# Optimization experiments

Measured on AMD Instinct MI355X. Metric: run time of the kernel, lower is better.

## Reference

```python
import jax, jax.numpy as jnp
import numpy as np

B, C2D, C3D, NC = 8, 256, 512, 128
H = W = 64
T = H3 = W3 = 16


def setup_inputs() -> dict:
    key = jax.random.key(0)
    ks = jax.random.split(key, 12)
    s = 0.02
    return {
        "features_2d": jax.random.normal(ks[0], (B, C2D, H, W), jnp.float32),
        "features_3d": jax.random.normal(ks[1], (B, C3D, T, H3, W3), jnp.float32),
        "Wq": jax.random.normal(ks[2], (NC, C2D), jnp.float32) * s,
        "bq": jax.random.normal(ks[3], (NC,), jnp.float32) * s,
        "Wk": jax.random.normal(ks[4], (NC, C3D), jnp.float32) * s,
        "bk": jax.random.normal(ks[5], (NC,), jnp.float32) * s,
        "Wv": jax.random.normal(ks[6], (NC, C3D), jnp.float32) * s,
        "bv": jax.random.normal(ks[7], (NC,), jnp.float32) * s,
        "Wo": jax.random.normal(ks[8], (C2D, NC), jnp.float32) * s,
        "bo": jax.random.normal(ks[9], (C2D,), jnp.float32) * s,
        "Wps": jax.random.normal(ks[10], (C2D, C2D, 3, 3), jnp.float32) * s,
        "bps": jax.random.normal(ks[11], (C2D,), jnp.float32) * s,
    }


def reference(features_2d, features_3d, Wq, bq, Wk, bk, Wv, bv, Wo, bo, Wps, bps):
    # 1x1 conv Q over 2D features: [B, NC, H*W] -> [B, N2d, NC]
    Q = jnp.einsum("bchw,oc->bohw", features_2d, Wq) + bq[None, :, None, None]
    Q = Q.reshape(B, NC, H * W).transpose(0, 2, 1)          # [B, N2d, NC]
    # 1x1 conv K/V over 3D features (no pooling: H3 <= max_height_3d)
    K = jnp.einsum("bcthw,oc->bothw", features_3d, Wk) + bk[None, :, None, None, None]
    V = jnp.einsum("bcthw,oc->bothw", features_3d, Wv) + bv[None, :, None, None, None]
    K = K.reshape(B, NC, T * H3 * W3)                        # [B, NC, N3d]
    V = V.reshape(B, NC, T * H3 * W3).transpose(0, 2, 1)     # [B, N3d, NC]
    # full non-local attention (no 1/sqrt(d) scaling, matching the torch code)
    att = jnp.einsum("bnc,bcm->bnm", Q, K)                   # [B, N2d, N3d]
    att = jax.nn.softmax(att, axis=-1)
    out = jnp.einsum("bnm,bmc->bnc", att, V)                 # [B, N2d, NC]
    out = out.transpose(0, 2, 1).reshape(B, NC, H, W)
    # 1x1 output conv back to channels_2d
    out = jnp.einsum("bchw,oc->bohw", out, Wo) + bo[None, :, None, None]
    # residual add + 3x3 post-sum conv
    x = features_2d + out
    y = jax.lax.conv_general_dilated(
        x, Wps, window_strides=(1, 1), padding="SAME",
        dimension_numbers=("NCHW", "OIHW", "NCHW"))
    return y + bps[None, :, None, None]
```

## Files before the change

kernel.cpp:

```cpp
#include <hip/hip_runtime.h>
#include <cstdint>

#define NB  8
#define C2  256
#define C3  512
#define NCH 128
#define NN2 4096
#define NN3 4096

using f4 = float4;
typedef float f32x16 __attribute__((ext_vector_type(16)));
typedef __bf16 bf16x8 __attribute__((ext_vector_type(8)));

union FragU {
    uint4    q;
    uint32_t u[4];
    bf16x8   v;
};

__device__ __forceinline__ void fma4(float* acc, float a, const f4 w) {
    acc[0] = fmaf(a, w.x, acc[0]);
    acc[1] = fmaf(a, w.y, acc[1]);
    acc[2] = fmaf(a, w.z, acc[2]);
    acc[3] = fmaf(a, w.w, acc[3]);
}

__device__ __forceinline__ unsigned short f2bf(float f) {
    uint32_t u = __float_as_uint(f);
    u += 0x7fffu + ((u >> 16) & 1u);
    return (unsigned short)(u >> 16);
}
__device__ __forceinline__ float bf2f(unsigned short h) {
    return __uint_as_float(((uint32_t)h) << 16);
}
__device__ __forceinline__ uint32_t pkbf(float lo, float hi) {
    union { __bf16 h[2]; uint32_t u; } t;
    t.h[0] = (__bf16)lo;
    t.h[1] = (__bf16)hi;
    return t.u;
}

__global__ __launch_bounds__(256) void wprep(const float* __restrict__ Wps,
                                             unsigned short* __restrict__ Wb) {
    int idx = blockIdx.x * 256 + threadIdx.x;
    int t = idx >> 16;
    int r = idx & 65535;
    int co = r >> 8, ci = r & 255;
    Wb[idx] = f2bf(Wps[((size_t)(co * 256 + ci)) * 9 + t]);
}

__global__ __launch_bounds__(256) void proj_q(const float* __restrict__ f2d,
                                              const float* __restrict__ Wq,
                                              const float* __restrict__ bq,
                                              unsigned short* __restrict__ Q) {
    __shared__ __align__(16) float As[32 * 68];
    __shared__ __align__(16) float Ws[32 * 132];
    const int tid = threadIdx.x;
    const int b  = blockIdx.x >> 6;
    const int n0 = (blockIdx.x & 63) << 6;
    const int tx = tid & 15, ty = tid >> 4;
    float acc[4][2][4];
#pragma unroll
    for (int i = 0; i < 4; i++)
#pragma unroll
        for (int v = 0; v < 2; v++)
#pragma unroll
            for (int u = 0; u < 4; u++) acc[i][v][u] = 0.f;
    const float* Ab = f2d + (size_t)b * C2 * NN2 + n0;
    for (int k0 = 0; k0 < C2; k0 += 32) {
#pragma unroll
        for (int i = 0; i < 2; i++) {
            int cidx = tid + 256 * i;
            int kk = cidx >> 4, noff = (cidx & 15) << 2;
            *(f4*)(As + kk * 68 + noff) = *(const f4*)(Ab + (size_t)(k0 + kk) * NN2 + noff);
        }
#pragma unroll
        for (int i = 0; i < 4; i++) {
            int cidx = tid + 256 * i;
            int cc = cidx >> 3, koff = (cidx & 7) << 2;
            f4 w = *(const f4*)(Wq + cc * C2 + k0 + koff);
            Ws[(koff + 0) * 132 + cc] = w.x;
            Ws[(koff + 1) * 132 + cc] = w.y;
            Ws[(koff + 2) * 132 + cc] = w.z;
            Ws[(koff + 3) * 132 + cc] = w.w;
        }
        __syncthreads();
#pragma unroll 8
        for (int kk = 0; kk < 32; kk++) {
            f4 a4 = *(const f4*)(As + kk * 68 + 4 * ty);
            f4 w0 = *(const f4*)(Ws + kk * 132 + 4 * tx);
            f4 w1 = *(const f4*)(Ws + kk * 132 + 4 * tx + 64);
            float av[4] = {a4.x, a4.y, a4.z, a4.w};
#pragma unroll
            for (int i = 0; i < 4; i++) { fma4(acc[i][0], av[i], w0); fma4(acc[i][1], av[i], w1); }
        }
        __syncthreads();
    }
    f4 b0 = *(const f4*)(bq + 4 * tx);
    f4 b1 = *(const f4*)(bq + 4 * tx + 64);
    float ba[2][4] = {{b0.x, b0.y, b0.z, b0.w}, {b1.x, b1.y, b1.z, b1.w}};
#pragma unroll
    for (int i = 0; i < 4; i++) {
        unsigned short* row = Q + ((size_t)b * NN2 + n0 + 4 * ty + i) * NCH;
#pragma unroll
        for (int v = 0; v < 2; v++) {
            ushort4 r;
            r.x = f2bf(acc[i][v][0] + ba[v][0]);
            r.y = f2bf(acc[i][v][1] + ba[v][1]);
            r.z = f2bf(acc[i][v][2] + ba[v][2]);
            r.w = f2bf(acc[i][v][3] + ba[v][3]);
            *(ushort4*)(row + 4 * tx + 64 * v) = r;
        }
    }
}

__global__ __launch_bounds__(256) void proj_kv(const float* __restrict__ f3d,
                                               const float* __restrict__ Wk,
                                               const float* __restrict__ bk,
                                               const float* __restrict__ Wv,
                                               const float* __restrict__ bv,
                                               unsigned short* __restrict__ K,
                                               unsigned short* __restrict__ Vt) {
    __shared__ __align__(16) float smem[2176 + 4224 + 4224];
    float* As  = smem;
    float* Wks = smem + 2176;
    float* Wvs = smem + 2176 + 4224;
    const int tid = threadIdx.x;
    const int b  = blockIdx.x >> 6;
    const int n0 = (blockIdx.x & 63) << 6;
    const int tx = tid & 15, ty = tid >> 4;
    float acck[4][2][4], accv[4][2][4];
#pragma unroll
    for (int i = 0; i < 4; i++)
#pragma unroll
        for (int v = 0; v < 2; v++)
#pragma unroll
            for (int u = 0; u < 4; u++) { acck[i][v][u] = 0.f; accv[i][v][u] = 0.f; }
    const float* Ab = f3d + (size_t)b * C3 * NN3 + n0;
    for (int k0 = 0; k0 < C3; k0 += 32) {
#pragma unroll
        for (int i = 0; i < 2; i++) {
            int cidx = tid + 256 * i;
            int kk = cidx >> 4, noff = (cidx & 15) << 2;
            *(f4*)(As + kk * 68 + noff) = *(const f4*)(Ab + (size_t)(k0 + kk) * NN3 + noff);
        }
#pragma unroll
        for (int i = 0; i < 4; i++) {
            int cidx = tid + 256 * i;
            int cc = cidx >> 3, koff = (cidx & 7) << 2;
            f4 wkv = *(const f4*)(Wk + cc * C3 + k0 + koff);
            Wks[(koff + 0) * 132 + cc] = wkv.x;
            Wks[(koff + 1) * 132 + cc] = wkv.y;
            Wks[(koff + 2) * 132 + cc] = wkv.z;
            Wks[(koff + 3) * 132 + cc] = wkv.w;
            f4 wvv = *(const f4*)(Wv + cc * C3 + k0 + koff);
            Wvs[(koff + 0) * 132 + cc] = wvv.x;
            Wvs[(koff + 1) * 132 + cc] = wvv.y;
            Wvs[(koff + 2) * 132 + cc] = wvv.z;
            Wvs[(koff + 3) * 132 + cc] = wvv.w;
        }
        __syncthreads();
#pragma unroll 4
        for (int kk = 0; kk < 32; kk++) {
            f4 a4  = *(const f4*)(As + kk * 68 + 4 * ty);
            f4 k0v = *(const f4*)(Wks + kk * 132 + 4 * tx);
            f4 k1v = *(const f4*)(Wks + kk * 132 + 4 * tx + 64);
            f4 v0v = *(const f4*)(Wvs + kk * 132 + 4 * tx);
            f4 v1v = *(const f4*)(Wvs + kk * 132 + 4 * tx + 64);
            float av[4] = {a4.x, a4.y, a4.z, a4.w};
#pragma unroll
            for (int i = 0; i < 4; i++) {
                fma4(acck[i][0], av[i], k0v); fma4(acck[i][1], av[i], k1v);
                fma4(accv[i][0], av[i], v0v); fma4(accv[i][1], av[i], v1v);
            }
        }
        __syncthreads();
    }
    f4 bk0 = *(const f4*)(bk + 4 * tx);
    f4 bk1 = *(const f4*)(bk + 4 * tx + 64);
    f4 bv0 = *(const f4*)(bv + 4 * tx);
    f4 bv1 = *(const f4*)(bv + 4 * tx + 64);
    float bka[2][4] = {{bk0.x, bk0.y, bk0.z, bk0.w}, {bk1.x, bk1.y, bk1.z, bk1.w}};
    float bva[2][4] = {{bv0.x, bv0.y, bv0.z, bv0.w}, {bv1.x, bv1.y, bv1.z, bv1.w}};
#pragma unroll
    for (int i = 0; i < 4; i++) {
        unsigned short* row = K + ((size_t)b * NN3 + n0 + 4 * ty + i) * NCH;
#pragma unroll
        for (int v = 0; v < 2; v++) {
            ushort4 r;
            r.x = f2bf(acck[i][v][0] + bka[v][0]);
            r.y = f2bf(acck[i][v][1] + bka[v][1]);
            r.z = f2bf(acck[i][v][2] + bka[v][2]);
            r.w = f2bf(acck[i][v][3] + bka[v][3]);
            *(ushort4*)(row + 4 * tx + 64 * v) = r;
        }
    }
    unsigned short* vt = (unsigned short*)smem;
#pragma unroll
    for (int i = 0; i < 4; i++) {
        int ml = 4 * ty + i;
#pragma unroll
        for (int v = 0; v < 2; v++)
#pragma unroll
            for (int u = 0; u < 4; u++) {
                int c = 4 * tx + 64 * v + u;
                vt[c * 72 + ml] = f2bf(accv[i][v][u] + bva[v][u]);
            }
    }
    __syncthreads();
#pragma unroll
    for (int j = 0; j < 4; j++) {
        int idx = tid + 256 * j;
        int c = idx >> 3, gm = idx & 7;
        uint4 d = *(const uint4*)(vt + c * 72 + gm * 8);
        *(uint4*)(Vt + ((size_t)b * NCH + c) * NN3 + n0 + gm * 8) = d;
    }
}

__global__ __launch_bounds__(128, 1) void attn(const unsigned short* __restrict__ Qg,
                                               const unsigned short* __restrict__ Kg,
                                               const unsigned short* __restrict__ Vtg,
                                               unsigned short* __restrict__ AO) {
    __shared__ __align__(16) unsigned short Ks[2][64 * 128];
    __shared__ __align__(16) unsigned short Vs[2][128 * 64];
    const int tid = threadIdx.x;
    const int b  = blockIdx.x >> 6;
    const int qc = blockIdx.x & 63;
    const int lane = tid & 63;
    const int wid = tid >> 6;
    const int i31 = lane & 31;
    const int h   = lane >> 5;
    const int q0w = qc * 64 + wid * 32;

    uint4 qf[8];
    const unsigned short* Qrow = Qg + ((size_t)b * NN2 + q0w + i31) * NCH;
#pragma unroll
    for (int dc = 0; dc < 8; dc++) qf[dc] = *(const uint4*)(Qrow + dc * 16 + h * 8);

    f32x16 o[4];
#pragma unroll
    for (int cf = 0; cf < 4; cf++)
#pragma unroll
        for (int r = 0; r < 16; r++) o[cf][r] = 0.f;
    float m_run = -3.0e38f, l_run = 0.f;

    const unsigned short* Kb = Kg  + (size_t)b * NN3 * NCH;
    const unsigned short* Vb = Vtg + (size_t)b * NCH * NN3;

    uint4 kst[8], vst[8];
#pragma unroll
    for (int j = 0; j < 8; j++) {
        int idx = tid + 128 * j;
        int key = idx >> 4, g = idx & 15;
        kst[j] = *(const uint4*)(Kb + (size_t)key * NCH + g * 8);
        int c = idx >> 3, gm = idx & 7;
        vst[j] = *(const uint4*)(Vb + (size_t)c * NN3 + gm * 8);
    }
#pragma unroll
    for (int j = 0; j < 8; j++) {
        int idx = tid + 128 * j;
        int key = idx >> 4, g = idx & 15;
        *(uint4*)(&Ks[0][key * 128 + ((g ^ (key & 7)) * 8)]) = kst[j];
        int c = idx >> 3, gm = idx & 7;
        *(uint4*)(&Vs[0][c * 64 + ((gm ^ (c & 7)) * 8)]) = vst[j];
    }
    __syncthreads();

    int buf = 0;
    for (int t = 0; t < 64; t++) {
        const bool more = (t + 1 < 64);
        const int m0n = more ? (t + 1) * 64 : 0;
        if (more) {
#pragma unroll
            for (int j = 0; j < 8; j++) {
                int idx = tid + 128 * j;
                int key = idx >> 4, g = idx & 15;
                kst[j] = *(const uint4*)(Kb + (size_t)(m0n + key) * NCH + g * 8);
                int c = idx >> 3, gm = idx & 7;
                vst[j] = *(const uint4*)(Vb + (size_t)c * NN3 + m0n + gm * 8);
            }
        }
        f32x16 sacc[2];
#pragma unroll
        for (int kf = 0; kf < 2; kf++)
#pragma unroll
            for (int r = 0; r < 16; r++) sacc[kf][r] = 0.f;
#pragma unroll
        for (int dc = 0; dc < 8; dc++) {
            FragU bq; bq.q = qf[dc];
#pragma unroll
            for (int kf = 0; kf < 2; kf++) {
                FragU ak;
                ak.q = *(const uint4*)(&Ks[buf][(kf * 32 + i31) * 128 + (((2 * dc + h) ^ (i31 & 7)) * 8)]);
                sacc[kf] = __builtin_amdgcn_mfma_f32_32x32x16_bf16(ak.v, bq.v, sacc[kf], 0, 0, 0);
            }
        }
        float tmax = -3.0e38f;
#pragma unroll
        for (int kf = 0; kf < 2; kf++)
#pragma unroll
            for (int r = 0; r < 16; r++) tmax = fmaxf(tmax, sacc[kf][r]);
        tmax = fmaxf(tmax, __shfl_xor(tmax, 32, 64));
        if (__any(tmax > m_run)) {
            float newm = fmaxf(m_run, tmax);
            float scale = __expf(m_run - newm);
            m_run = newm;
            l_run *= scale;
#pragma unroll
            for (int reg = 0; reg < 16; reg++) {
                int qrow = (reg & 3) + 8 * (reg >> 2) + 4 * h;
                float sc = __shfl(scale, qrow, 64);
#pragma unroll
                for (int cf = 0; cf < 4; cf++) o[cf][reg] *= sc;
            }
        }
        float psum = 0.f;
#pragma unroll
        for (int kf = 0; kf < 2; kf++)
#pragma unroll
            for (int r = 0; r < 16; r++) {
                float e = __expf(sacc[kf][r] - m_run);
                sacc[kf][r] = e;
                psum += e;
            }
        psum += __shfl_xor(psum, 32, 64);
        l_run += psum;
        uint32_t pk[2][8];
#pragma unroll
        for (int kf = 0; kf < 2; kf++)
#pragma unroll
            for (int j = 0; j < 8; j++) pk[kf][j] = pkbf(sacc[kf][2 * j], sacc[kf][2 * j + 1]);
#pragma unroll
        for (int kc = 0; kc < 4; kc++) {
            const int kf = kc >> 1, kcp = kc & 1;
            uint32_t own_lo  = pk[kf][4 * kcp + 0];
            uint32_t own_lo2 = pk[kf][4 * kcp + 1];
            uint32_t own_hi  = pk[kf][4 * kcp + 2];
            uint32_t own_hi2 = pk[kf][4 * kcp + 3];
            uint32_t send1 = h ? own_lo  : own_hi;
            uint32_t send2 = h ? own_lo2 : own_hi2;
            uint32_t recv1 = (uint32_t)__shfl_xor((int)send1, 32, 64);
            uint32_t recv2 = (uint32_t)__shfl_xor((int)send2, 32, 64);
            FragU pa;
            pa.u[0] = h ? recv1 : own_lo;
            pa.u[1] = h ? recv2 : own_lo2;
            pa.u[2] = h ? own_hi  : recv1;
            pa.u[3] = h ? own_hi2 : recv2;
#pragma unroll
            for (int cf = 0; cf < 4; cf++) {
                FragU vbf;
                vbf.q = *(const uint4*)(&Vs[buf][(cf * 32 + i31) * 64 + (((2 * kc + h) ^ (i31 & 7)) * 8)]);
                o[cf] = __builtin_amdgcn_mfma_f32_32x32x16_bf16(pa.v, vbf.v, o[cf], 0, 0, 0);
            }
        }
        if (more) {
#pragma unroll
            for (int j = 0; j < 8; j++) {
                int idx = tid + 128 * j;
                int key = idx >> 4, g = idx & 15;
                *(uint4*)(&Ks[buf ^ 1][key * 128 + ((g ^ (key & 7)) * 8)]) = kst[j];
                int c = idx >> 3, gm = idx & 7;
                *(uint4*)(&Vs[buf ^ 1][c * 64 + ((gm ^ (c & 7)) * 8)]) = vst[j];
            }
        }
        __syncthreads();
        buf ^= 1;
    }
    float inv = 1.0f / l_run;
#pragma unroll
    for (int reg = 0; reg < 16; reg++) {
        int qrow = (reg & 3) + 8 * (reg >> 2) + 4 * h;
        float iv = __shfl(inv, qrow, 64);
        unsigned short* row = AO + ((size_t)b * NN2 + q0w + qrow) * NCH;
#pragma unroll
        for (int cf = 0; cf < 4; cf++) row[cf * 32 + i31] = f2bf(o[cf][reg] * iv);
    }
}

__global__ __launch_bounds__(256) void outproj(const unsigned short* __restrict__ AO,
                                               const float* __restrict__ Wo,
                                               const float* __restrict__ bo,
                                               const float* __restrict__ f2d,
                                               unsigned short* __restrict__ Xn) {
    __shared__ __align__(16) float smem[2176 + 4224];
    float* Wt = smem;
    float* At = smem + 2176;
    const int tid = threadIdx.x;
    const int b = blockIdx.x >> 7;
    const int r = blockIdx.x & 127;
    const int co0 = (r >> 5) << 6;
    const int n0  = (r & 31) << 7;
    const int tx = tid & 15, ty = tid >> 4;
    float acc[4][2][4];
#pragma unroll
    for (int i = 0; i < 4; i++)
#pragma unroll
        for (int v = 0; v < 2; v++)
#pragma unroll
            for (int u = 0; u < 4; u++) acc[i][v][u] = 0.f;
    for (int c0 = 0; c0 < NCH; c0 += 32) {
#pragma unroll
        for (int i = 0; i < 2; i++) {
            int cidx = tid + 256 * i;
            int cr = cidx >> 3, koff = (cidx & 7) << 2;
            f4 w = *(const f4*)(Wo + (co0 + cr) * NCH + c0 + koff);
            Wt[(koff + 0) * 68 + cr] = w.x;
            Wt[(koff + 1) * 68 + cr] = w.y;
            Wt[(koff + 2) * 68 + cr] = w.z;
            Wt[(koff + 3) * 68 + cr] = w.w;
        }
#pragma unroll
        for (int i = 0; i < 4; i++) {
            int cidx = tid + 256 * i;
            int nn = cidx >> 3, koff = (cidx & 7) << 2;
            ushort4 a4 = *(const ushort4*)(AO + ((size_t)b * NN2 + n0 + nn) * NCH + c0 + koff);
            At[(koff + 0) * 132 + nn] = bf2f(a4.x);
            At[(koff + 1) * 132 + nn] = bf2f(a4.y);
            At[(koff + 2) * 132 + nn] = bf2f(a4.z);
            At[(koff + 3) * 132 + nn] = bf2f(a4.w);
        }
        __syncthreads();
#pragma unroll 8
        for (int kk = 0; kk < 32; kk++) {
            f4 a4 = *(const f4*)(Wt + kk * 68 + 4 * ty);
            f4 x0 = *(const f4*)(At + kk * 132 + 4 * tx);
            f4 x1 = *(const f4*)(At + kk * 132 + 4 * tx + 64);
            float av[4] = {a4.x, a4.y, a4.z, a4.w};
#pragma unroll
            for (int i = 0; i < 4; i++) { fma4(acc[i][0], av[i], x0); fma4(acc[i][1], av[i], x1); }
        }
        __syncthreads();
    }
    unsigned short* tb = (unsigned short*)smem;
#pragma unroll
    for (int i = 0; i < 4; i++) {
        int co = co0 + 4 * ty + i;
        float bias = bo[co];
        const size_t rowb = ((size_t)b * C2 + co) * NN2 + n0;
#pragma unroll
        for (int v = 0; v < 2; v++) {
            size_t pidx = rowb + 4 * tx + 64 * v;
            f4 f = *(const f4*)(f2d + pidx);
            int nl = 4 * tx + 64 * v;
            tb[(nl + 0) * 72 + 4 * ty + i] = f2bf(acc[i][v][0] + bias + f.x);
            tb[(nl + 1) * 72 + 4 * ty + i] = f2bf(acc[i][v][1] + bias + f.y);
            tb[(nl + 2) * 72 + 4 * ty + i] = f2bf(acc[i][v][2] + bias + f.z);
            tb[(nl + 3) * 72 + 4 * ty + i] = f2bf(acc[i][v][3] + bias + f.w);
        }
    }
    __syncthreads();
#pragma unroll
    for (int k = 0; k < 4; k++) {
        int unit = tid + 256 * k;
        int nl = unit >> 3, cc = unit & 7;
        uint4 d = *(const uint4*)(tb + nl * 72 + cc * 8);
        *(uint4*)(Xn + ((size_t)b * NN2 + n0 + nl) * C2 + co0 + cc * 8) = d;
    }
}

__global__ __launch_bounds__(256) void conv3x3(const unsigned short* __restrict__ Xn,
                                               const unsigned short* __restrict__ Wb,
                                               const float* __restrict__ bps,
                                               float* __restrict__ Y) {
    __shared__ __align__(16) unsigned short Xs[680 * 8];
    const int tid = threadIdx.x;
    const int b  = blockIdx.x >> 6;
    const int r  = blockIdx.x & 63;
    const int ct = r >> 4;
    const int pt = r & 15;
    const int px0 = (pt & 1) << 5;
    const int py0 = (pt >> 1) << 3;
    const int w    = tid >> 6;
    const int lane = tid & 63;
    const int i31  = lane & 31;
    const int h    = lane >> 5;
    const int co0  = ct << 6;

    f32x16 acc[2][2];
#pragma unroll
    for (int ch = 0; ch < 2; ch++)
#pragma unroll
        for (int pf = 0; pf < 2; pf++)
#pragma unroll
            for (int q = 0; q < 16; q++) acc[ch][pf][q] = 0.f;

    const unsigned short* Xb = Xn + (size_t)b * NN2 * C2;

    uint4 sreg[3];
    int su[3], sy[3], sx[3], sh[3];
#pragma unroll
    for (int k = 0; k < 3; k++) {
        int u = tid + 256 * k;
        su[k] = (u < 680);
        int pix = u >> 1;
        sy[k] = pix / 34;
        sx[k] = pix - sy[k] * 34;
        sh[k] = u & 1;
    }

    auto stage_load = [&](int ci0) {
#pragma unroll
        for (int k = 0; k < 3; k++) {
            uint4 z = {0, 0, 0, 0};
            if (su[k]) {
                int gy = py0 - 1 + sy[k];
                int gx = px0 - 1 + sx[k];
                if ((unsigned)gy < 64u && (unsigned)gx < 64u)
                    z = *(const uint4*)(Xb + ((size_t)(gy * 64 + gx)) * C2 + ci0 + 8 * sh[k]);
            }
            sreg[k] = z;
        }
    };
    auto stage_write = [&]() {
#pragma unroll
        for (int k = 0; k < 3; k++) {
            if (su[k]) {
                int slot = (sy[k] * 2 + sh[k]) * 34 + sx[k];
                *(uint4*)(&Xs[slot * 8]) = sreg[k];
            }
        }
    };

    stage_load(0);
    stage_write();
    __syncthreads();

    for (int c = 0; c < 16; c++) {
        const int ci0n = (c + 1) * 16;
        if (c + 1 < 16) stage_load(ci0n);
        const int ci0 = c * 16;
#pragma unroll
        for (int t = 0; t < 9; t++) {
            const int dy = t / 3, dx = t - dy * 3;
            FragU a0, a1;
            a0.q = *(const uint4*)(Wb + ((size_t)(t * 256 + co0 + i31)) * 256 + ci0 + 8 * h);
            a1.q = *(const uint4*)(Wb + ((size_t)(t * 256 + co0 + 32 + i31)) * 256 + ci0 + 8 * h);
#pragma unroll
            for (int pf = 0; pf < 2; pf++) {
                const int yl = 2 * w + pf;
                FragU bx;
                bx.q = *(const uint4*)(&Xs[(((yl + dy) * 2 + h) * 34 + i31 + dx) * 8]);
                acc[0][pf] = __builtin_amdgcn_mfma_f32_32x32x16_bf16(a0.v, bx.v, acc[0][pf], 0, 0, 0);
                acc[1][pf] = __builtin_amdgcn_mfma_f32_32x32x16_bf16(a1.v, bx.v, acc[1][pf], 0, 0, 0);
            }
        }
        __syncthreads();
        if (c + 1 < 16) stage_write();
        __syncthreads();
    }

#pragma unroll
    for (int ch = 0; ch < 2; ch++)
#pragma unroll
        for (int pf = 0; pf < 2; pf++) {
            const int y = py0 + 2 * w + pf;
            const int x = px0 + i31;
#pragma unroll
            for (int q = 0; q < 16; q++) {
                int co = co0 + ch * 32 + (q & 3) + 8 * (q >> 2) + 4 * h;
                Y[(((size_t)b * C2 + co) * 64 + y) * 64 + x] = acc[ch][pf][q] + bps[co];
            }
        }
}

extern "C" void kernel_launch(void* const* d_in, const int* in_sizes, int n_in,
                              void* d_out, int out_size, void* d_ws, size_t ws_size,
                              hipStream_t stream) {
    const float* f2d = (const float*)d_in[0];
    const float* f3d = (const float*)d_in[1];
    const float* Wq  = (const float*)d_in[2];
    const float* bq  = (const float*)d_in[3];
    const float* Wk  = (const float*)d_in[4];
    const float* bk  = (const float*)d_in[5];
    const float* Wv  = (const float*)d_in[6];
    const float* bv  = (const float*)d_in[7];
    const float* Wo  = (const float*)d_in[8];
    const float* bo  = (const float*)d_in[9];
    const float* Wps = (const float*)d_in[10];
    const float* bps = (const float*)d_in[11];
    float* Y = (float*)d_out;

    unsigned short* Qb  = (unsigned short*)d_ws;
    unsigned short* Kb  = Qb + 4194304;
    unsigned short* Vtb = Kb + 4194304;
    unsigned short* AOb = Vtb + 4194304;
    unsigned short* Xnb = AOb + 4194304;
    unsigned short* Wbb = Xnb + 8388608;

    dim3 blk(256);
    wprep   <<<dim3(2304), blk, 0, stream>>>(Wps, Wbb);
    proj_q  <<<dim3(512),  blk, 0, stream>>>(f2d, Wq, bq, Qb);
    proj_kv <<<dim3(512),  blk, 0, stream>>>(f3d, Wk, bk, Wv, bv, Kb, Vtb);
    attn    <<<dim3(512),  dim3(128), 0, stream>>>(Qb, Kb, Vtb, AOb);
    outproj <<<dim3(1024), blk, 0, stream>>>(AOb, Wo, bo, f2d, Xnb);
    conv3x3 <<<dim3(512),  blk, 0, stream>>>(Xnb, Wbb, bps, Y);
}
```

Measured before the change: 534.4 us.

## Use bf16 MFMA for Q/K/V projections and split attention keys across wave pairs

Replaces the fp32 FMA Q and K/V projection kernels with bf16 MFMA kernels, fed by a new weight-conversion pre-pass and double-buffered LDS staging. The attention kernel moves to 256 threads: two wave pairs each handle half of the key range and are merged at the end with a log-sum-exp combine through shared memory. It also adds s_setprio around the MFMA sections. The aim is to cut projection ALU time and raise attention occupancy and parallelism, at the cost of bf16 rounding of the projection inputs and an extra merge step.

```diff
diff --git a/kernel.cpp b/kernel.cpp
--- a/kernel.cpp
+++ b/kernel.cpp
@@ -18,26 +18,25 @@
     bf16x8   v;
 };
 
+__device__ __forceinline__ unsigned short f2bf(float f) {
+    uint32_t u = __float_as_uint(f);
+    u += 0x7fffu + ((u >> 16) & 1u);
+    return (unsigned short)(u >> 16);
+}
+__device__ __forceinline__ float bf2f(unsigned short h) {
+    return __uint_as_float(((uint32_t)h) << 16);
+}
+__device__ __forceinline__ uint32_t pkbf(float lo, float hi) {
+    union { __bf16 h[2]; uint32_t u; } t;
+    t.h[0] = (__bf16)lo;
+    t.h[1] = (__bf16)hi;
+    return t.u;
+}
 __device__ __forceinline__ void fma4(float* acc, float a, const f4 w) {
     acc[0] = fmaf(a, w.x, acc[0]);
     acc[1] = fmaf(a, w.y, acc[1]);
     acc[2] = fmaf(a, w.z, acc[2]);
     acc[3] = fmaf(a, w.w, acc[3]);
-}
-
-__device__ __forceinline__ unsigned short f2bf(float f) {
-    uint32_t u = __float_as_uint(f);
-    u += 0x7fffu + ((u >> 16) & 1u);
-    return (unsigned short)(u >> 16);
-}
-__device__ __forceinline__ float bf2f(unsigned short h) {
-    return __uint_as_float(((uint32_t)h) << 16);
-}
-__device__ __forceinline__ uint32_t pkbf(float lo, float hi) {
-    union { __bf16 h[2]; uint32_t u; } t;
-    t.h[0] = (__bf16)lo;
-    t.h[1] = (__bf16)hi;
-    return t.u;
 }
 
 __global__ __launch_bounds__(256) void wprep(const float* __restrict__ Wps,
@@ -49,188 +48,205 @@
     Wb[idx] = f2bf(Wps[((size_t)(co * 256 + ci)) * 9 + t]);
 }
 
+__global__ __launch_bounds__(256) void wprep2(const float* __restrict__ Wq,
+                                              const float* __restrict__ Wk,
+                                              const float* __restrict__ Wv,
+                                              unsigned short* __restrict__ Wqb,
+                                              unsigned short* __restrict__ Wkb,
+                                              unsigned short* __restrict__ Wvb) {
+    int idx = blockIdx.x * 256 + threadIdx.x;
+    if (idx < 32768)        Wqb[idx]          = f2bf(Wq[idx]);
+    else if (idx < 98304)   Wkb[idx - 32768]  = f2bf(Wk[idx - 32768]);
+    else                    Wvb[idx - 98304]  = f2bf(Wv[idx - 98304]);
+}
+
 __global__ __launch_bounds__(256) void proj_q(const float* __restrict__ f2d,
-                                              const float* __restrict__ Wq,
+                                              const unsigned short* __restrict__ Wqb,
                                               const float* __restrict__ bq,
                                               unsigned short* __restrict__ Q) {
-    __shared__ __align__(16) float As[32 * 68];
-    __shared__ __align__(16) float Ws[32 * 132];
+    __shared__ __align__(16) unsigned short Xs[2][128 * 40];
     const int tid = threadIdx.x;
-    const int b  = blockIdx.x >> 6;
-    const int n0 = (blockIdx.x & 63) << 6;
-    const int tx = tid & 15, ty = tid >> 4;
-    float acc[4][2][4];
-#pragma unroll
-    for (int i = 0; i < 4; i++)
-#pragma unroll
-        for (int v = 0; v < 2; v++)
-#pragma unroll
-            for (int u = 0; u < 4; u++) acc[i][v][u] = 0.f;
-    const float* Ab = f2d + (size_t)b * C2 * NN2 + n0;
-    for (int k0 = 0; k0 < C2; k0 += 32) {
-#pragma unroll
-        for (int i = 0; i < 2; i++) {
-            int cidx = tid + 256 * i;
-            int kk = cidx >> 4, noff = (cidx & 15) << 2;
-            *(f4*)(As + kk * 68 + noff) = *(const f4*)(Ab + (size_t)(k0 + kk) * NN2 + noff);
-        }
-#pragma unroll
-        for (int i = 0; i < 4; i++) {
-            int cidx = tid + 256 * i;
-            int cc = cidx >> 3, koff = (cidx & 7) << 2;
-            f4 w = *(const f4*)(Wq + cc * C2 + k0 + koff);
-            Ws[(koff + 0) * 132 + cc] = w.x;
-            Ws[(koff + 1) * 132 + cc] = w.y;
-            Ws[(koff + 2) * 132 + cc] = w.z;
-            Ws[(koff + 3) * 132 + cc] = w.w;
-        }
+    const int b  = blockIdx.x >> 5;
+    const int n0 = (blockIdx.x & 31) << 7;
+    const int wn = tid >> 6;
+    const int lane = tid & 63;
+    const int i31 = lane & 31;
+    const int h   = lane >> 5;
+    const int kp = tid >> 4;
+    const int nc = tid & 15;
+
+    f32x16 aQ[4];
+#pragma unroll
+    for (int cf = 0; cf < 4; cf++)
+#pragma unroll
+        for (int r = 0; r < 16; r++) aQ[cf][r] = 0.f;
+
+    float xlo[8], xhi[8];
+    auto LOADC = [&](int k0) {
+        const float* r0 = f2d + ((size_t)b * C2 + k0 + 2 * kp) * NN2 + n0 + nc;
+        const float* r1 = r0 + NN2;
+#pragma unroll
+        for (int i = 0; i < 8; i++) { xlo[i] = r0[16 * i]; xhi[i] = r1[16 * i]; }
+    };
+    auto WRITEC = [&](int bi) {
+        unsigned short* X = Xs[bi];
+#pragma unroll
+        for (int i = 0; i < 8; i++)
+            *(uint32_t*)&X[(nc + 16 * i) * 40 + 2 * kp] = pkbf(xlo[i], xhi[i]);
+    };
+
+    LOADC(0); WRITEC(0); __syncthreads();
+    int cur = 0;
+    for (int c = 0; c < 8; c++) {
+        if (c + 1 < 8) LOADC((c + 1) * 32);
+        const int k0 = c * 32;
+        FragU xf[2];
+        xf[0].q = *(const uint4*)&Xs[cur][(wn * 32 + i31) * 40 + h * 8];
+        xf[1].q = *(const uint4*)&Xs[cur][(wn * 32 + i31) * 40 + 16 + h * 8];
+#pragma unroll
+        for (int ks = 0; ks < 2; ks++) {
+            const int ko = k0 + ks * 16 + h * 8;
+#pragma unroll
+            for (int cf = 0; cf < 4; cf++) {
+                FragU wq;
+                wq.q = *(const uint4*)&Wqb[(size_t)(cf * 32 + i31) * 256 + ko];
+                aQ[cf] = __builtin_amdgcn_mfma_f32_32x32x16_bf16(wq.v, xf[ks].v, aQ[cf], 0, 0, 0);
+            }
+        }
+        if (c + 1 < 8) WRITEC(cur ^ 1);
         __syncthreads();
-#pragma unroll 8
-        for (int kk = 0; kk < 32; kk++) {
-            f4 a4 = *(const f4*)(As + kk * 68 + 4 * ty);
-            f4 w0 = *(const f4*)(Ws + kk * 132 + 4 * tx);
-            f4 w1 = *(const f4*)(Ws + kk * 132 + 4 * tx + 64);
-            float av[4] = {a4.x, a4.y, a4.z, a4.w};
-#pragma unroll
-            for (int i = 0; i < 4; i++) { fma4(acc[i][0], av[i], w0); fma4(acc[i][1], av[i], w1); }
-        }
-        __syncthreads();
-    }
-    f4 b0 = *(const f4*)(bq + 4 * tx);
-    f4 b1 = *(const f4*)(bq + 4 * tx + 64);
-    float ba[2][4] = {{b0.x, b0.y, b0.z, b0.w}, {b1.x, b1.y, b1.z, b1.w}};
-#pragma unroll
-    for (int i = 0; i < 4; i++) {
-        unsigned short* row = Q + ((size_t)b * NN2 + n0 + 4 * ty + i) * NCH;
-#pragma unroll
-        for (int v = 0; v < 2; v++) {
-            ushort4 r;
-            r.x = f2bf(acc[i][v][0] + ba[v][0]);
-            r.y = f2bf(acc[i][v][1] + ba[v][1]);
-            r.z = f2bf(acc[i][v][2] + ba[v][2]);
-            r.w = f2bf(acc[i][v][3] + ba[v][3]);
-            *(ushort4*)(row + 4 * tx + 64 * v) = r;
-        }
-    }
+        cur ^= 1;
+    }
+    const int nQ = n0 + wn * 32 + i31;
+    unsigned short* Qrow = Q + ((size_t)b * NN2 + nQ) * NCH;
+#pragma unroll
+    for (int cf = 0; cf < 4; cf++)
+#pragma unroll
+        for (int tq = 0; tq < 4; tq++) {
+            int c0 = cf * 32 + 8 * tq + 4 * h;
+            f4 bb = *(const f4*)(bq + c0);
+            ushort4 s;
+            s.x = f2bf(aQ[cf][4 * tq + 0] + bb.x);
+            s.y = f2bf(aQ[cf][4 * tq + 1] + bb.y);
+            s.z = f2bf(aQ[cf][4 * tq + 2] + bb.z);
+            s.w = f2bf(aQ[cf][4 * tq + 3] + bb.w);
+            *(ushort4*)(Qrow + c0) = s;
+        }
 }
 
 __global__ __launch_bounds__(256) void proj_kv(const float* __restrict__ f3d,
-                                               const float* __restrict__ Wk,
+                                               const unsigned short* __restrict__ Wkb,
                                                const float* __restrict__ bk,
-                                               const float* __restrict__ Wv,
+                                               const unsigned short* __restrict__ Wvb,
                                                const float* __restrict__ bv,
                                                unsigned short* __restrict__ K,
                                                unsigned short* __restrict__ Vt) {
-    __shared__ __align__(16) float smem[2176 + 4224 + 4224];
-    float* As  = smem;
-    float* Wks = smem + 2176;
-    float* Wvs = smem + 2176 + 4224;
+    __shared__ __align__(16) unsigned short Xs[2][128 * 40];
     const int tid = threadIdx.x;
-    const int b  = blockIdx.x >> 6;
-    const int n0 = (blockIdx.x & 63) << 6;
-    const int tx = tid & 15, ty = tid >> 4;
-    float acck[4][2][4], accv[4][2][4];
-#pragma unroll
-    for (int i = 0; i < 4; i++)
-#pragma unroll
-        for (int v = 0; v < 2; v++)
-#pragma unroll
-            for (int u = 0; u < 4; u++) { acck[i][v][u] = 0.f; accv[i][v][u] = 0.f; }
-    const float* Ab = f3d + (size_t)b * C3 * NN3 + n0;
-    for (int k0 = 0; k0 < C3; k0 += 32) {
-#pragma unroll
-        for (int i = 0; i < 2; i++) {
-            int cidx = tid + 256 * i;
-            int kk = cidx >> 4, noff = (cidx & 15) << 2;
-            *(f4*)(As + kk * 68 + noff) = *(const f4*)(Ab + (size_t)(k0 + kk) * NN3 + noff);
-        }
-#pragma unroll
-        for (int i = 0; i < 4; i++) {
-            int cidx = tid + 256 * i;
-            int cc = cidx >> 3, koff = (cidx & 7) << 2;
-            f4 wkv = *(const f4*)(Wk + cc * C3 + k0 + koff);
-            Wks[(koff + 0) * 132 + cc] = wkv.x;
-            Wks[(koff + 1) * 132 + cc] = wkv.y;
-            Wks[(koff + 2) * 132 + cc] = wkv.z;
-            Wks[(koff + 3) * 132 + cc] = wkv.w;
-            f4 wvv = *(const f4*)(Wv + cc * C3 + k0 + koff);
-            Wvs[(koff + 0) * 132 + cc] = wvv.x;
-            Wvs[(koff + 1) * 132 + cc] = wvv.y;
-            Wvs[(koff + 2) * 132 + cc] = wvv.z;
-            Wvs[(koff + 3) * 132 + cc] = wvv.w;
-        }
+    const int b  = blockIdx.x >> 5;
+    const int n0 = (blockIdx.x & 31) << 7;
+    const int wn = tid >> 6;
+    const int lane = tid & 63;
+    const int i31 = lane & 31;
+    const int h   = lane >> 5;
+    const int kp = tid >> 4;
+    const int nc = tid & 15;
+
+    f32x16 aK[4], aV[4];
+#pragma unroll
+    for (int cf = 0; cf < 4; cf++)
+#pragma unroll
+        for (int r = 0; r < 16; r++) { aK[cf][r] = 0.f; aV[cf][r] = 0.f; }
+
+    float xlo[8], xhi[8];
+    auto LOADC = [&](int k0) {
+        const float* r0 = f3d + ((size_t)b * C3 + k0 + 2 * kp) * NN3 + n0 + nc;
+        const float* r1 = r0 + NN3;
+#pragma unroll
+        for (int i = 0; i < 8; i++) { xlo[i] = r0[16 * i]; xhi[i] = r1[16 * i]; }
+    };
+    auto WRITEC = [&](int bi) {
+        unsigned short* X = Xs[bi];
+#pragma unroll
+        for (int i = 0; i < 8; i++)
+            *(uint32_t*)&X[(nc + 16 * i) * 40 + 2 * kp] = pkbf(xlo[i], xhi[i]);
+    };
+
+    LOADC(0); WRITEC(0); __syncthreads();
+    int cur = 0;
+    for (int c = 0; c < 16; c++) {
+        if (c + 1 < 16) LOADC((c + 1) * 32);
+        const int k0 = c * 32;
+        FragU xf[2];
+        xf[0].q = *(const uint4*)&Xs[cur][(wn * 32 + i31) * 40 + h * 8];
+        xf[1].q = *(const uint4*)&Xs[cur][(wn * 32 + i31) * 40 + 16 + h * 8];
+#pragma unroll
+        for (int ks = 0; ks < 2; ks++) {
+            const int ko = k0 + ks * 16 + h * 8;
+#pragma unroll
+            for (int cf = 0; cf < 4; cf++) {
+                FragU wk, wv;
+                wk.q = *(const uint4*)&Wkb[(size_t)(cf * 32 + i31) * 512 + ko];
+                wv.q = *(const uint4*)&Wvb[(size_t)(cf * 32 + i31) * 512 + ko];
+                aK[cf] = __builtin_amdgcn_mfma_f32_32x32x16_bf16(wk.v, xf[ks].v, aK[cf], 0, 0, 0);
+                aV[cf] = __builtin_amdgcn_mfma_f32_32x32x16_bf16(xf[ks].v, wv.v, aV[cf], 0, 0, 0);
+            }
+        }
+        if (c + 1 < 16) WRITEC(cur ^ 1);
         __syncthreads();
-#pragma unroll 4
-        for (int kk = 0; kk < 32; kk++) {
-            f4 a4  = *(const f4*)(As + kk * 68 + 4 * ty);
-            f4 k0v = *(const f4*)(Wks + kk * 132 + 4 * tx);
-            f4 k1v = *(const f4*)(Wks + kk * 132 + 4 * tx + 64);
-            f4 v0v = *(const f4*)(Wvs + kk * 132 + 4 * tx);
-            f4 v1v = *(const f4*)(Wvs + kk * 132 + 4 * tx + 64);
-            float av[4] = {a4.x, a4.y, a4.z, a4.w};
-#pragma unroll
-            for (int i = 0; i < 4; i++) {
-                fma4(acck[i][0], av[i], k0v); fma4(acck[i][1], av[i], k1v);
-                fma4(accv[i][0], av[i], v0v); fma4(accv[i][1], av[i], v1v);
-            }
-        }
-        __syncthreads();
-    }
-    f4 bk0 = *(const f4*)(bk + 4 * tx);
-    f4 bk1 = *(const f4*)(bk + 4 * tx + 64);
-    f4 bv0 = *(const f4*)(bv + 4 * tx);
-    f4 bv1 = *(const f4*)(bv + 4 * tx + 64);
-    float bka[2][4] = {{bk0.x, bk0.y, bk0.z, bk0.w}, {bk1.x, bk1.y, bk1.z, bk1.w}};
-    float bva[2][4] = {{bv0.x, bv0.y, bv0.z, bv0.w}, {bv1.x, bv1.y, bv1.z, bv1.w}};
-#pragma unroll
-    for (int i = 0; i < 4; i++) {
-        unsigned short* row = K + ((size_t)b * NN3 + n0 + 4 * ty + i) * NCH;
-#pragma unroll
-        for (int v = 0; v < 2; v++) {
-            ushort4 r;
-            r.x = f2bf(acck[i][v][0] + bka[v][0]);
-            r.y = f2bf(acck[i][v][1] + bka[v][1]);
-            r.z = f2bf(acck[i][v][2] + bka[v][2]);
-            r.w = f2bf(acck[i][v][3] + bka[v][3]);
-            *(ushort4*)(row + 4 * tx + 64 * v) = r;
-        }
-    }
-    unsigned short* vt = (unsigned short*)smem;
-#pragma unroll
-    for (int i = 0; i < 4; i++) {
-        int ml = 4 * ty + i;
-#pragma unroll
-        for (int v = 0; v < 2; v++)
-#pragma unroll
-            for (int u = 0; u < 4; u++) {
-                int c = 4 * tx + 64 * v + u;
-                vt[c * 72 + ml] = f2bf(accv[i][v][u] + bva[v][u]);
-            }
-    }
-    __syncthreads();
-#pragma unroll
-    for (int j = 0; j < 4; j++) {
-        int idx = tid + 256 * j;
-        int c = idx >> 3, gm = idx & 7;
-        uint4 d = *(const uint4*)(vt + c * 72 + gm * 8);
-        *(uint4*)(Vt + ((size_t)b * NCH + c) * NN3 + n0 + gm * 8) = d;
-    }
-}
-
-__global__ __launch_bounds__(128, 1) void attn(const unsigned short* __restrict__ Qg,
-                                               const unsigned short* __restrict__ Kg,
-                                               const unsigned short* __restrict__ Vtg,
-                                               unsigned short* __restrict__ AO) {
-    __shared__ __align__(16) unsigned short Ks[2][64 * 128];
-    __shared__ __align__(16) unsigned short Vs[2][128 * 64];
+        cur ^= 1;
+    }
+    const int nK = n0 + wn * 32 + i31;
+    unsigned short* Krow = K + ((size_t)b * NN3 + nK) * NCH;
+#pragma unroll
+    for (int cf = 0; cf < 4; cf++)
+#pragma unroll
+        for (int tq = 0; tq < 4; tq++) {
+            int c0 = cf * 32 + 8 * tq + 4 * h;
+            f4 bb = *(const f4*)(bk + c0);
+            ushort4 s;
+            s.x = f2bf(aK[cf][4 * tq + 0] + bb.x);
+            s.y = f2bf(aK[cf][4 * tq + 1] + bb.y);
+            s.z = f2bf(aK[cf][4 * tq + 2] + bb.z);
+            s.w = f2bf(aK[cf][4 * tq + 3] + bb.w);
+            *(ushort4*)(Krow + c0) = s;
+        }
+#pragma unroll
+    for (int cf = 0; cf < 4; cf++) {
+        const int cV = cf * 32 + i31;
+        const float bvv = bv[cV];
+        unsigned short* Vrow = Vt + ((size_t)b * NCH + cV) * NN3;
+#pragma unroll
+        for (int tq = 0; tq < 4; tq++) {
+            int nq = n0 + wn * 32 + 8 * tq + 4 * h;
+            ushort4 s;
+            s.x = f2bf(aV[cf][4 * tq + 0] + bvv);
+            s.y = f2bf(aV[cf][4 * tq + 1] + bvv);
+            s.z = f2bf(aV[cf][4 * tq + 2] + bvv);
+            s.w = f2bf(aV[cf][4 * tq + 3] + bvv);
+            *(ushort4*)(Vrow + nq) = s;
+        }
+    }
+}
+
+__global__ __launch_bounds__(256) void attn(const unsigned short* __restrict__ Qg,
+                                            const unsigned short* __restrict__ Kg,
+                                            const unsigned short* __restrict__ Vtg,
+                                            unsigned short* __restrict__ AO) {
+    __shared__ __align__(16) unsigned short smem[32768];
     const int tid = threadIdx.x;
     const int b  = blockIdx.x >> 6;
     const int qc = blockIdx.x & 63;
+    const int wid = tid >> 6;
     const int lane = tid & 63;
-    const int wid = tid >> 6;
     const int i31 = lane & 31;
     const int h   = lane >> 5;
-    const int q0w = qc * 64 + wid * 32;
+    const int p    = wid >> 1;
+    const int tid2 = tid & 127;
+    const int q0w  = qc * 64 + (wid & 1) * 32;
+    const int kbase = p * 2048;
+    unsigned short* Ksp = smem + p * 16384;
+    unsigned short* Vsp = smem + p * 16384 + 8192;
 
     uint4 qf[8];
     const unsigned short* Qrow = Qg + ((size_t)b * NN2 + q0w + i31) * NCH;
@@ -247,59 +263,54 @@
     const unsigned short* Kb = Kg  + (size_t)b * NN3 * NCH;
     const unsigned short* Vb = Vtg + (size_t)b * NCH * NN3;
 
-    uint4 kst[8], vst[8];
-#pragma unroll
-    for (int j = 0; j < 8; j++) {
-        int idx = tid + 128 * j;
+    uint4 kst[4], vst[4];
+#pragma unroll
+    for (int j = 0; j < 4; j++) {
+        int idx = tid2 + 128 * j;
         int key = idx >> 4, g = idx & 15;
-        kst[j] = *(const uint4*)(Kb + (size_t)key * NCH + g * 8);
-        int c = idx >> 3, gm = idx & 7;
-        vst[j] = *(const uint4*)(Vb + (size_t)c * NN3 + gm * 8);
-    }
-#pragma unroll
-    for (int j = 0; j < 8; j++) {
-        int idx = tid + 128 * j;
+        kst[j] = *(const uint4*)(Kb + (size_t)(kbase + key) * NCH + g * 8);
+        int c = idx >> 2, gm = idx & 3;
+        vst[j] = *(const uint4*)(Vb + (size_t)c * NN3 + kbase + gm * 8);
+    }
+#pragma unroll
+    for (int j = 0; j < 4; j++) {
+        int idx = tid2 + 128 * j;
         int key = idx >> 4, g = idx & 15;
-        *(uint4*)(&Ks[0][key * 128 + ((g ^ (key & 7)) * 8)]) = kst[j];
-        int c = idx >> 3, gm = idx & 7;
-        *(uint4*)(&Vs[0][c * 64 + ((gm ^ (c & 7)) * 8)]) = vst[j];
+        *(uint4*)(&Ksp[key * 128 + ((g ^ (key & 7)) * 8)]) = kst[j];
+        int c = idx >> 2, gm = idx & 3;
+        *(uint4*)(&Vsp[c * 32 + ((gm ^ (c & 3)) * 8)]) = vst[j];
     }
     __syncthreads();
 
     int buf = 0;
     for (int t = 0; t < 64; t++) {
         const bool more = (t + 1 < 64);
-        const int m0n = more ? (t + 1) * 64 : 0;
         if (more) {
-#pragma unroll
-            for (int j = 0; j < 8; j++) {
-                int idx = tid + 128 * j;
+            const int m0n = kbase + (t + 1) * 32;
+#pragma unroll
+            for (int j = 0; j < 4; j++) {
+                int idx = tid2 + 128 * j;
                 int key = idx >> 4, g = idx & 15;
                 kst[j] = *(const uint4*)(Kb + (size_t)(m0n + key) * NCH + g * 8);
-                int c = idx >> 3, gm = idx & 7;
+                int c = idx >> 2, gm = idx & 3;
                 vst[j] = *(const uint4*)(Vb + (size_t)c * NN3 + m0n + gm * 8);
             }
         }
-        f32x16 sacc[2];
-#pragma unroll
-        for (int kf = 0; kf < 2; kf++)
-#pragma unroll
-            for (int r = 0; r < 16; r++) sacc[kf][r] = 0.f;
+        f32x16 sacc;
+#pragma unroll
+        for (int r = 0; r < 16; r++) sacc[r] = 0.f;
+        __builtin_amdgcn_s_setprio(1);
 #pragma unroll
         for (int dc = 0; dc < 8; dc++) {
             FragU bq; bq.q = qf[dc];
-#pragma unroll
-            for (int kf = 0; kf < 2; kf++) {
-                FragU ak;
-                ak.q = *(const uint4*)(&Ks[buf][(kf * 32 + i31) * 128 + (((2 * dc + h) ^ (i31 & 7)) * 8)]);
-                sacc[kf] = __builtin_amdgcn_mfma_f32_32x32x16_bf16(ak.v, bq.v, sacc[kf], 0, 0, 0);
-            }
-        }
+            FragU ak;
+            ak.q = *(const uint4*)(&Ksp[buf * 4096 + i31 * 128 + (((2 * dc + h) ^ (i31 & 7)) * 8)]);
+            sacc = __builtin_amdgcn_mfma_f32_32x32x16_bf16(ak.v, bq.v, sacc, 0, 0, 0);
+        }
+        __builtin_amdgcn_s_setprio(0);
         float tmax = -3.0e38f;
 #pragma unroll
-        for (int kf = 0; kf < 2; kf++)
-#pragma unroll
-            for (int r = 0; r < 16; r++) tmax = fmaxf(tmax, sacc[kf][r]);
+        for (int r = 0; r < 16; r++) tmax = fmaxf(tmax, sacc[r]);
         tmax = fmaxf(tmax, __shfl_xor(tmax, 32, 64));
         if (__any(tmax > m_run)) {
             float newm = fmaxf(m_run, tmax);
@@ -316,27 +327,23 @@
         }
         float psum = 0.f;
 #pragma unroll
-        for (int kf = 0; kf < 2; kf++)
-#pragma unroll
-            for (int r = 0; r < 16; r++) {
-                float e = __expf(sacc[kf][r] - m_run);
-                sacc[kf][r] = e;
-                psum += e;
-            }
+        for (int r = 0; r < 16; r++) {
+            float e = __expf(sacc[r] - m_run);
+            sacc[r] = e;
+            psum += e;
+        }
         psum += __shfl_xor(psum, 32, 64);
         l_run += psum;
-        uint32_t pk[2][8];
-#pragma unroll
-        for (int kf = 0; kf < 2; kf++)
-#pragma unroll
-            for (int j = 0; j < 8; j++) pk[kf][j] = pkbf(sacc[kf][2 * j], sacc[kf][2 * j + 1]);
-#pragma unroll
-        for (int kc = 0; kc < 4; kc++) {
-            const int kf = kc >> 1, kcp = kc & 1;
-            uint32_t own_lo  = pk[kf][4 * kcp + 0];
-            uint32_t own_lo2 = pk[kf][4 * kcp + 1];
-            uint32_t own_hi  = pk[kf][4 * kcp + 2];
-            uint32_t own_hi2 = pk[kf][4 * kcp + 3];
+        uint32_t pk[8];
+#pragma unroll
+        for (int j = 0; j < 8; j++) pk[j] = pkbf(sacc[2 * j], sacc[2 * j + 1]);
+        __builtin_amdgcn_s_setprio(1);
+#pragma unroll
+        for (int kc = 0; kc < 2; kc++) {
+            uint32_t own_lo  = pk[4 * kc + 0];
+            uint32_t own_lo2 = pk[4 * kc + 1];
+            uint32_t own_hi  = pk[4 * kc + 2];
+            uint32_t own_hi2 = pk[4 * kc + 3];
             uint32_t send1 = h ? own_lo  : own_hi;
             uint32_t send2 = h ? own_lo2 : own_hi2;
             uint32_t recv1 = (uint32_t)__shfl_xor((int)send1, 32, 64);
@@ -349,31 +356,61 @@
 #pragma unroll
             for (int cf = 0; cf < 4; cf++) {
                 FragU vbf;
-                vbf.q = *(const uint4*)(&Vs[buf][(cf * 32 + i31) * 64 + (((2 * kc + h) ^ (i31 & 7)) * 8)]);
+                vbf.q = *(const uint4*)(&Vsp[buf * 4096 + (cf * 32 + i31) * 32 + (((2 * kc + h) ^ (i31 & 3)) * 8)]);
                 o[cf] = __builtin_amdgcn_mfma_f32_32x32x16_bf16(pa.v, vbf.v, o[cf], 0, 0, 0);
             }
         }
+        __builtin_amdgcn_s_setprio(0);
         if (more) {
 #pragma unroll
-            for (int j = 0; j < 8; j++) {
-                int idx = tid + 128 * j;
+            for (int j = 0; j < 4; j++) {
+                int idx = tid2 + 128 * j;
                 int key = idx >> 4, g = idx & 15;
-                *(uint4*)(&Ks[buf ^ 1][key * 128 + ((g ^ (key & 7)) * 8)]) = kst[j];
-                int c = idx >> 3, gm = idx & 7;
-                *(uint4*)(&Vs[buf ^ 1][c * 64 + ((gm ^ (c & 7)) * 8)]) = vst[j];
+                *(uint4*)(&Ksp[(buf ^ 1) * 4096 + key * 128 + ((g ^ (key & 7)) * 8)]) = kst[j];
+                int c = idx >> 2, gm = idx & 3;
+                *(uint4*)(&Vsp[(buf ^ 1) * 4096 + c * 32 + ((gm ^ (c & 3)) * 8)]) = vst[j];
             }
         }
         __syncthreads();
         buf ^= 1;
     }
-    float inv = 1.0f / l_run;
-#pragma unroll
-    for (int reg = 0; reg < 16; reg++) {
-        int qrow = (reg & 3) + 8 * (reg >> 2) + 4 * h;
-        float iv = __shfl(inv, qrow, 64);
-        unsigned short* row = AO + ((size_t)b * NN2 + q0w + qrow) * NCH;
-#pragma unroll
-        for (int cf = 0; cf < 4; cf++) row[cf * 32 + i31] = f2bf(o[cf][reg] * iv);
+    float* mo = (float*)smem;
+    const int s = wid & 1;
+    if (wid >= 2) {
+        float* mos = mo + s * 4224;
+#pragma unroll
+        for (int cf = 0; cf < 4; cf++)
+#pragma unroll
+            for (int reg = 0; reg < 16; reg++) {
+                int qrow = (reg & 3) + 8 * (reg >> 2) + 4 * h;
+                mos[qrow * 132 + cf * 32 + i31] = o[cf][reg];
+            }
+        float* ml = mo + 8448;
+        if (h == 0) { ml[s * 64 + i31] = m_run; ml[s * 64 + 32 + i31] = l_run; }
+    }
+    __syncthreads();
+    if (wid < 2) {
+        float* mos = mo + s * 4224;
+        float* ml  = mo + 8448;
+        float m2 = ml[s * 64 + i31];
+        float l2 = ml[s * 64 + 32 + i31];
+        float M  = fmaxf(m_run, m2);
+        float a0 = __expf(m_run - M);
+        float a2 = __expf(m2 - M);
+        float inv = 1.0f / (a0 * l_run + a2 * l2);
+#pragma unroll
+        for (int reg = 0; reg < 16; reg++) {
+            int qrow = (reg & 3) + 8 * (reg >> 2) + 4 * h;
+            float a0q = __shfl(a0, qrow, 64);
+            float a2q = __shfl(a2, qrow, 64);
+            float ivq = __shfl(inv, qrow, 64);
+            unsigned short* row = AO + ((size_t)b * NN2 + q0w + qrow) * NCH;
+#pragma unroll
+            for (int cf = 0; cf < 4; cf++) {
+                float val = (a0q * o[cf][reg] + a2q * mos[qrow * 132 + cf * 32 + i31]) * ivq;
+                row[cf * 32 + i31] = f2bf(val);
+            }
+        }
     }
 }
 
@@ -526,8 +563,7 @@
     __syncthreads();
 
     for (int c = 0; c < 16; c++) {
-        const int ci0n = (c + 1) * 16;
-        if (c + 1 < 16) stage_load(ci0n);
+        if (c + 1 < 16) stage_load((c + 1) * 16);
         const int ci0 = c * 16;
 #pragma unroll
         for (int t = 0; t < 9; t++) {
@@ -586,12 +622,16 @@
     unsigned short* AOb = Vtb + 4194304;
     unsigned short* Xnb = AOb + 4194304;
     unsigned short* Wbb = Xnb + 8388608;
+    unsigned short* Wqb = Wbb + 589824;
+    unsigned short* Wkb = Wqb + 32768;
+    unsigned short* Wvb = Wkb + 65536;
 
     dim3 blk(256);
     wprep   <<<dim3(2304), blk, 0, stream>>>(Wps, Wbb);
-    proj_q  <<<dim3(512),  blk, 0, stream>>>(f2d, Wq, bq, Qb);
-    proj_kv <<<dim3(512),  blk, 0, stream>>>(f3d, Wk, bk, Wv, bv, Kb, Vtb);
-    attn    <<<dim3(512),  dim3(128), 0, stream>>>(Qb, Kb, Vtb, AOb);
+    wprep2  <<<dim3(640),  blk, 0, stream>>>(Wq, Wk, Wv, Wqb, Wkb, Wvb);
+    proj_q  <<<dim3(256),  blk, 0, stream>>>(f2d, Wqb, bq, Qb);
+    proj_kv <<<dim3(256),  blk, 0, stream>>>(f3d, Wkb, bk, Wvb, bv, Kb, Vtb);
+    attn    <<<dim3(512),  blk, 0, stream>>>(Qb, Kb, Vtb, AOb);
     outproj <<<dim3(1024), blk, 0, stream>>>(AOb, Wo, bo, f2d, Xnb);
     conv3x3 <<<dim3(512),  blk, 0, stream>>>(Xnb, Wbb, bps, Y);
 }
```

Result: slower. 612.5 us (+14.6%).
